# Kernel optimization log

Hardware: AMD Instinct MI355X
Metric: run time of the kernel (lower is better)

The kernel has to match this reference:

```python
import jax, jax.numpy as jnp
import numpy as np
from jax import lax

B, N, C, H = 8, 1024, 384, 6
D = C // H
SCALE = D ** -0.5
EPS = 1e-5


def setup_inputs() -> dict:
    key = jax.random.key(0)
    ks = jax.random.split(key, 10)
    s = 0.02
    return {
        "x": jax.random.normal(ks[0], (B, N, C), jnp.float32),
        "w_qkv": jax.random.normal(ks[1], (3 * C, C), jnp.float32) * s,
        "w_proj": jax.random.normal(ks[2], (C, C), jnp.float32) * s,
        "b_proj": jax.random.normal(ks[3], (C,), jnp.float32) * s,
        "w_kq": jax.random.normal(ks[4], (H, 1, 3, 3), jnp.float32) * 0.1,   # depthwise (groups=H)
        "b_kq": jax.random.normal(ks[5], (H,), jnp.float32) * 0.1,
        "w_head": jax.random.normal(ks[6], (H, H, 1, 1), jnp.float32) * 0.1,  # 1x1 head-mixing conv
        "b_head": jax.random.normal(ks[7], (H,), jnp.float32) * 0.1,
        "gn_w": jnp.ones((H,), jnp.float32),
        "gn_b": jnp.zeros((H,), jnp.float32),
    }


def reference(x, w_qkv, w_proj, b_proj, w_kq, b_kq, w_head, b_head, gn_w, gn_b):
    # qkv projection (torch Linear: y = x @ W.T)
    qkv = (x @ w_qkv.T).reshape(B, N, 3, H, D).transpose(2, 0, 3, 1, 4)  # [3,B,H,N,D]
    q, k, v = qkv[0], qkv[1], qkv[2]

    # attention logits [B,H,N,N]
    logits = jnp.einsum("bhnd,bhmd->bhnm", q, k) * SCALE

    # depthwise (groups=H) 3x3 conv over the NxN logit map
    logits = lax.conv_general_dilated(
        logits, w_kq, window_strides=(1, 1), padding=((1, 1), (1, 1)),
        dimension_numbers=("NCHW", "OIHW", "NCHW"), feature_group_count=H,
    ) + b_kq[None, :, None, None]

    attn = jax.nn.softmax(logits, axis=-1)

    # 1x1 conv mixing heads
    attn = jnp.einsum("oh,bhnm->bonm", w_head[:, :, 0, 0], attn) + b_head[None, :, None, None]

    # GroupNorm(num_groups=H, channels=H): per (b, head) stats over NxN
    mean = attn.mean(axis=(2, 3), keepdims=True)
    var = ((attn - mean) ** 2).mean(axis=(2, 3), keepdims=True)
    attn = (attn - mean) * lax.rsqrt(var + EPS)
    attn = attn * gn_w[None, :, None, None] + gn_b[None, :, None, None]

    out = jnp.einsum("bhnm,bhmd->bhnd", attn, v)
    out = out.transpose(0, 2, 1, 3).reshape(B, N, C)
    return out @ w_proj.T + b_proj
```

## Files before the change

### kernel.cpp

```cpp
#include <hip/hip_runtime.h>

typedef unsigned short u16;
typedef __attribute__((ext_vector_type(8))) short short8;
typedef __attribute__((ext_vector_type(4))) float f32x4;

#define MFMA(a, b, c) __builtin_amdgcn_mfma_f32_16x16x32_bf16((a), (b), (c), 0, 0, 0)

__device__ inline float bf2f(u16 u) {
  union { unsigned int i; float f; } w; w.i = ((unsigned int)u) << 16; return w.f;
}
__device__ inline u16 f2bf(float x) {
  union { float f; unsigned int i; } u; u.f = x;
  unsigned int r = u.i + 0x7fffu + ((u.i >> 16) & 1u);
  return (u16)(r >> 16);
}
__device__ inline unsigned int pk2(float a, float b) {
  return (unsigned int)f2bf(a) | ((unsigned int)f2bf(b) << 16);
}
__device__ inline void unpack8(uint4 v, float* f) {
  union { unsigned int i; float g; } c;
  c.i = v.x << 16;          f[0] = c.g;
  c.i = v.x & 0xffff0000u;  f[1] = c.g;
  c.i = v.y << 16;          f[2] = c.g;
  c.i = v.y & 0xffff0000u;  f[3] = c.g;
  c.i = v.z << 16;          f[4] = c.g;
  c.i = v.z & 0xffff0000u;  f[5] = c.g;
  c.i = v.w << 16;          f[6] = c.g;
  c.i = v.w & 0xffff0000u;  f[7] = c.g;
}

static const size_t SZ_QKV = (size_t)48 * 1024 * 64 * 2;
static const size_t SZ_MAP = (size_t)48 * 1024 * 1024 * 2;
static const size_t OFF_Q  = 0;
static const size_t OFF_K  = OFF_Q + SZ_QKV;
static const size_t OFF_VT = OFF_K + SZ_QKV;
static const size_t OFF_S  = OFF_VT + SZ_QKV;
static const size_t OFF_UG = OFF_S;
static const size_t OFF_QM = OFF_S + SZ_MAP;
static const size_t OFF_OT = OFF_QM + SZ_MAP;
static const size_t OFF_ST = OFF_OT + SZ_QKV;
static const size_t OFF_CS = OFF_ST + 896;
static const size_t OFF_AD = OFF_CS + 12288;
static const size_t OFF_AL = OFF_AD + 12288;

__global__ __launch_bounds__(256, 3) void k_qkv(const float* __restrict__ x,
                                                const float* __restrict__ w,
                                                u16* __restrict__ qb,
                                                u16* __restrict__ kb,
                                                u16* __restrict__ vT,
                                                float* __restrict__ colsum) {
  __shared__ u16 SH[16384];
  u16* As = SH;
  u16* Bs = SH + 8192;
  const int t = threadIdx.x;
  const int m0 = blockIdx.x * 128;
  const int n0 = blockIdx.y * 128;
  const int wave = t >> 6, lane = t & 63;
  const int wm = (wave & 1) * 64, wn = (wave >> 1) * 64;
  const int fr = lane & 15;
  const int fk = (lane >> 4) * 8;
  f32x4 acc[4][4] = {};
  for (int k0 = 0; k0 < 384; k0 += 64) {
#pragma unroll
    for (int i = 0; i < 4; ++i) {
      int e = (i * 256 + t) * 8;
      int row = e >> 6, col = e & 63;
      const float* xp = &x[(size_t)(m0 + row) * 384 + k0 + col];
      const float* wp = &w[(size_t)(n0 + row) * 384 + k0 + col];
      float4 a0 = *(const float4*)xp, a1 = *(const float4*)(xp + 4);
      uint4 av; av.x = pk2(a0.x, a0.y); av.y = pk2(a0.z, a0.w);
      av.z = pk2(a1.x, a1.y); av.w = pk2(a1.z, a1.w);
      *(uint4*)&As[e] = av;
      float4 b0 = *(const float4*)wp, b1 = *(const float4*)(wp + 4);
      uint4 bv; bv.x = pk2(b0.x, b0.y); bv.y = pk2(b0.z, b0.w);
      bv.z = pk2(b1.x, b1.y); bv.w = pk2(b1.z, b1.w);
      *(uint4*)&Bs[e] = bv;
    }
    __syncthreads();
#pragma unroll
    for (int ks = 0; ks < 2; ++ks) {
      const int ko = ks * 32 + fk;
      short8 a[4], b[4];
#pragma unroll
      for (int mi = 0; mi < 4; ++mi) a[mi] = *(const short8*)&As[(wm + mi * 16 + fr) * 64 + ko];
#pragma unroll
      for (int ni = 0; ni < 4; ++ni) b[ni] = *(const short8*)&Bs[(wn + ni * 16 + fr) * 64 + ko];
#pragma unroll
      for (int mi = 0; mi < 4; ++mi)
#pragma unroll
        for (int ni = 0; ni < 4; ++ni) acc[mi][ni] = MFMA(a[mi], b[ni], acc[mi][ni]);
    }
    __syncthreads();
  }
  u16* st = &SH[wave * 4096];
  const int gcb = n0 + wn;
  const int s = gcb / 384;
  const int remb = gcb - s * 384;
  const int h = remb >> 6;
#pragma unroll
  for (int mi = 0; mi < 4; ++mi)
#pragma unroll
    for (int ni = 0; ni < 4; ++ni)
#pragma unroll
      for (int r = 0; r < 4; ++r) {
        int rl = mi * 16 + (lane >> 4) * 4 + r;
        int cl = ni * 16 + fr;
        u16 val = f2bf(acc[mi][ni][r]);
        if (s == 2) st[cl * 64 + rl] = val;
        else        st[rl * 64 + cl] = val;
      }
  const int gm0 = m0 + wm;
  const int b_ = gm0 >> 10;
  const size_t base = (size_t)(b_ * 6 + h) << 16;
  const int nloc = gm0 & 1023;
  const int r8 = lane >> 3, c8 = (lane & 7) * 8;
#pragma unroll
  for (int i = 0; i < 8; ++i) {
    int lrow = i * 8 + r8;
    uint4 v = *(const uint4*)&st[lrow * 64 + c8];
    if (s == 0)      *(uint4*)&qb[base + (size_t)(nloc + lrow) * 64 + c8] = v;
    else if (s == 1) *(uint4*)&kb[base + (size_t)(nloc + lrow) * 64 + c8] = v;
    else             *(uint4*)&vT[base + (size_t)lrow * 1024 + nloc + c8] = v;
  }
  if (s == 2) {
#pragma unroll
    for (int ni = 0; ni < 4; ++ni) {
      float p = 0.f;
#pragma unroll
      for (int mi = 0; mi < 4; ++mi)
#pragma unroll
        for (int r = 0; r < 4; ++r) p += bf2f(f2bf(acc[mi][ni][r]));
      p += __shfl_xor(p, 16, 64);
      p += __shfl_xor(p, 32, 64);
      if ((lane >> 4) == 0)
        atomicAdd(&colsum[(b_ * 6 + h) * 64 + ni * 16 + fr], p);
    }
  }
}

__global__ __launch_bounds__(256, 3) void k_qk(const u16* __restrict__ qb,
                                               const u16* __restrict__ kb,
                                               u16* __restrict__ S) {
  __shared__ u16 SH[16384];
  u16* As = SH;
  u16* Bs = SH + 8192;
  const int t = threadIdx.x;
  const int m0 = blockIdx.x * 128, n0 = blockIdx.y * 128;
  const int bh = blockIdx.z;
  const u16* A = qb + ((size_t)bh << 16);
  const u16* Bp = kb + ((size_t)bh << 16);
  const int wave = t >> 6, lane = t & 63;
  const int wm = (wave & 1) * 64, wn = (wave >> 1) * 64;
  const int fr = lane & 15;
  const int fk = (lane >> 4) * 8;
  f32x4 acc[4][4] = {};
#pragma unroll
  for (int i = 0; i < 4; ++i) {
    int e = (i * 256 + t) * 8;
    *(uint4*)&As[e] = *(const uint4*)&A[(size_t)m0 * 64 + e];
    *(uint4*)&Bs[e] = *(const uint4*)&Bp[(size_t)n0 * 64 + e];
  }
  __syncthreads();
#pragma unroll
  for (int ks = 0; ks < 2; ++ks) {
    const int ko = ks * 32 + fk;
    short8 a[4], b[4];
#pragma unroll
    for (int mi = 0; mi < 4; ++mi) a[mi] = *(const short8*)&As[(wm + mi * 16 + fr) * 64 + ko];
#pragma unroll
    for (int ni = 0; ni < 4; ++ni) b[ni] = *(const short8*)&Bs[(wn + ni * 16 + fr) * 64 + ko];
#pragma unroll
    for (int mi = 0; mi < 4; ++mi)
#pragma unroll
      for (int ni = 0; ni < 4; ++ni) acc[mi][ni] = MFMA(a[mi], b[ni], acc[mi][ni]);
  }
  __syncthreads();
  u16* st = &SH[wave * 4096];
#pragma unroll
  for (int mi = 0; mi < 4; ++mi)
#pragma unroll
    for (int ni = 0; ni < 4; ++ni)
#pragma unroll
      for (int r = 0; r < 4; ++r)
        st[(mi * 16 + (lane >> 4) * 4 + r) * 64 + ni * 16 + fr] = f2bf(acc[mi][ni][r] * 0.125f);
  const size_t sb = (size_t)bh << 20;
  const int grow0 = m0 + wm, gcol0 = n0 + wn;
  const int r8 = lane >> 3, c8 = (lane & 7) * 8;
#pragma unroll
  for (int i = 0; i < 8; ++i) {
    int lrow = i * 8 + r8;
    uint4 v = *(const uint4*)&st[lrow * 64 + c8];
    *(uint4*)&S[sb + (size_t)(grow0 + lrow) * 1024 + gcol0 + c8] = v;
  }
}

__global__ __launch_bounds__(256) void k_conv_softmax(const u16* __restrict__ S,
                                                      const float* __restrict__ w_kq,
                                                      u16* __restrict__ Qb) {
  __shared__ u16 Sr[10 * 1040];
  __shared__ float red[4];
  const int t = threadIdx.x;
  const int bh = blockIdx.y;
  const int h = bh % 6;
  const int r0 = blockIdx.x * 8;
  const u16* Sp = S + ((size_t)bh << 20);
  float wv[9];
#pragma unroll
  for (int i = 0; i < 9; ++i) wv[i] = w_kq[h * 9 + i];
  if (t < 10) { Sr[t * 1040 + 7] = 0; Sr[t * 1040 + 1032] = 0; }
#pragma unroll
  for (int c = 0; c < 5; ++c) {
    int e = (c * 256 + t) * 8;
    int i = e >> 10, col = e & 1023;
    int g = r0 - 1 + i;
    uint4 val = make_uint4(0u, 0u, 0u, 0u);
    if (g >= 0 && g < 1024) val = *(const uint4*)&Sp[(size_t)g * 1024 + col];
    *(uint4*)&Sr[i * 1040 + 8 + col] = val;
  }
  __syncthreads();
  const int half = t >> 7;
  const int lane = t & 63;
  const int m0 = (t & 127) * 8;
  for (int pass = 0; pass < 4; ++pass) {
    int rr = pass * 2 + half;
    float o8[8];
#pragma unroll
    for (int j = 0; j < 8; ++j) o8[j] = 0.f;
#pragma unroll
    for (int i = 0; i < 3; ++i) {
      const u16* rowp = &Sr[(rr + i) * 1040 + 8];
      float left = bf2f(rowp[m0 - 1]);
      float md[8];
      unpack8(*(const uint4*)&rowp[m0], md);
      float right = bf2f(rowp[m0 + 8]);
      float w0 = wv[i * 3 + 0], w1 = wv[i * 3 + 1], w2 = wv[i * 3 + 2];
      o8[0] += w0 * left + w1 * md[0] + w2 * md[1];
#pragma unroll
      for (int j = 1; j < 7; ++j) o8[j] += w0 * md[j - 1] + w1 * md[j] + w2 * md[j + 1];
      o8[7] += w0 * md[6] + w1 * md[7] + w2 * right;
    }
    float mx = o8[0];
#pragma unroll
    for (int j = 1; j < 8; ++j) mx = fmaxf(mx, o8[j]);
    for (int off = 32; off; off >>= 1) mx = fmaxf(mx, __shfl_xor(mx, off, 64));
    if (lane == 0) red[t >> 6] = mx;
    __syncthreads();
    float rmax = fmaxf(red[half * 2], red[half * 2 + 1]);
    __syncthreads();
    float e8[8], s = 0.f;
#pragma unroll
    for (int j = 0; j < 8; ++j) { e8[j] = __expf(o8[j] - rmax); s += e8[j]; }
    for (int off = 32; off; off >>= 1) s += __shfl_xor(s, off, 64);
    if (lane == 0) red[t >> 6] = s;
    __syncthreads();
    float rsum = red[half * 2] + red[half * 2 + 1];
    __syncthreads();
    float scale = 1024.f / rsum;
    unsigned int pk[4];
#pragma unroll
    for (int jj = 0; jj < 4; ++jj)
      pk[jj] = pk2(e8[2 * jj] * scale - 1.f, e8[2 * jj + 1] * scale - 1.f);
    int n = r0 + rr;
    *(uint4*)&Qb[((size_t)bh << 20) + (size_t)n * 1024 + m0] = make_uint4(pk[0], pk[1], pk[2], pk[3]);
  }
}

__global__ __launch_bounds__(256) void k_pvmix(const u16* __restrict__ Qm,
                                               const u16* __restrict__ vT,
                                               const float* __restrict__ wh,
                                               float* __restrict__ Ug,
                                               float* __restrict__ stats) {
  __shared__ u16 SH[2 * 64 * 72];
  u16* Am = SH;
  u16* Vm = SH + 64 * 72;
  const int t = threadIdx.x;
  const int n0 = blockIdx.x * 64;
  const int bo = blockIdx.y;
  const int b_ = bo / 6, o = bo - b_ * 6;
  const int wave = t >> 6, lane = t & 63;
  const int fr = lane & 15, quad = lane >> 4;
  const int srow = t >> 3, smg8 = (t & 7) * 8;
  float wo[6];
#pragma unroll
  for (int hh = 0; hh < 6; ++hh) wo[hh] = wh[o * 6 + hh];
  const size_t qbase = ((size_t)(b_ * 6)) << 20;
  const u16* vp = vT + ((size_t)bo << 16);
  uint4 qpre[2][6];
  uint4 vpre[2];
  {
    const int m = smg8;
#pragma unroll
    for (int i = 0; i < 2; ++i)
#pragma unroll
      for (int hh = 0; hh < 6; ++hh)
        qpre[i][hh] = *(const uint4*)&Qm[qbase + (((size_t)hh) << 20) +
                                         (size_t)(n0 + i * 32 + srow) * 1024 + m];
    vpre[0] = *(const uint4*)&vp[(size_t)srow * 1024 + m];
    vpre[1] = *(const uint4*)&vp[(size_t)(32 + srow) * 1024 + m];
  }
  f32x4 acc[4] = {};
  float s1 = 0.f, s2 = 0.f;
  for (int mc = 0; mc < 16; ++mc) {
    __syncthreads();
#pragma unroll
    for (int i = 0; i < 2; ++i) {
      float mix[8] = {0.f, 0.f, 0.f, 0.f, 0.f, 0.f, 0.f, 0.f};
#pragma unroll
      for (int hh = 0; hh < 6; ++hh) {
        float qf[8];
        unpack8(qpre[i][hh], qf);
        float w = wo[hh];
#pragma unroll
        for (int j = 0; j < 8; ++j) mix[j] += w * qf[j];
      }
#pragma unroll
      for (int j = 0; j < 8; ++j) { s1 += mix[j]; s2 += mix[j] * mix[j]; }
      uint4 pk4;
      pk4.x = pk2(mix[0], mix[1]); pk4.y = pk2(mix[2], mix[3]);
      pk4.z = pk2(mix[4], mix[5]); pk4.w = pk2(mix[6], mix[7]);
      *(uint4*)&Am[(i * 32 + srow) * 72 + smg8] = pk4;
    }
    *(uint4*)&Vm[srow * 72 + smg8] = vpre[0];
    *(uint4*)&Vm[(32 + srow) * 72 + smg8] = vpre[1];
    if (mc < 15) {
      const int m = (mc + 1) * 64 + smg8;
#pragma unroll
      for (int i = 0; i < 2; ++i)
#pragma unroll
        for (int hh = 0; hh < 6; ++hh)
          qpre[i][hh] = *(const uint4*)&Qm[qbase + (((size_t)hh) << 20) +
                                           (size_t)(n0 + i * 32 + srow) * 1024 + m];
      vpre[0] = *(const uint4*)&vp[(size_t)srow * 1024 + m];
      vpre[1] = *(const uint4*)&vp[(size_t)(32 + srow) * 1024 + m];
    }
    __syncthreads();
#pragma unroll
    for (int ks = 0; ks < 2; ++ks) {
      short8 a = *(const short8*)&Am[(wave * 16 + fr) * 72 + ks * 32 + quad * 8];
#pragma unroll
      for (int ni = 0; ni < 4; ++ni) {
        short8 b = *(const short8*)&Vm[(ni * 16 + fr) * 72 + ks * 32 + quad * 8];
        acc[ni] = MFMA(a, b, acc[ni]);
      }
    }
  }
  __syncthreads();
  float* FS = (float*)SH;
#pragma unroll
  for (int ni = 0; ni < 4; ++ni)
#pragma unroll
    for (int r = 0; r < 4; ++r)
      FS[(wave * 16 + quad * 4 + r) * 64 + ni * 16 + fr] = acc[ni][r];
  __syncthreads();
  float* Up = Ug + ((size_t)(bo * 1024 + n0)) * 64;
#pragma unroll
  for (int j = 0; j < 4; ++j) {
    int oo = j * 1024 + t * 4;
    *(float4*)&Up[oo] = *(const float4*)&FS[oo];
  }
  for (int off = 32; off; off >>= 1) {
    s1 += __shfl_xor(s1, off, 64);
    s2 += __shfl_xor(s2, off, 64);
  }
  if (lane == 0) {
    atomicAdd(&stats[bo * 2 + 0], s1);
    atomicAdd(&stats[bo * 2 + 1], s2);
  }
}

__global__ __launch_bounds__(256) void k_finalize(const float* __restrict__ stats,
                                                  const float* __restrict__ colsum,
                                                  const float* __restrict__ gn_w,
                                                  const float* __restrict__ gn_b,
                                                  float* __restrict__ addend,
                                                  float* __restrict__ alphaArr) {
  int gid = blockIdx.x * 256 + threadIdx.x;
  int bo = gid >> 6, d = gid & 63;
  int o = bo % 6;
  float s1 = stats[bo * 2], s2 = stats[bo * 2 + 1];
  const float inv = 1.f / 1048576.f;
  float mu = s1 * inv;
  float var = s2 * inv - mu * mu;
  float alpha = gn_w[o] * rsqrtf(var + 1e-5f * 1048576.f);
  float beta = gn_b[o] - alpha * mu;
  addend[gid] = beta * colsum[gid];
  if (d == 0) alphaArr[bo] = alpha;
}

__global__ __launch_bounds__(256) void k_apply(const float* __restrict__ Ug,
                                               const float* __restrict__ alphaArr,
                                               const float* __restrict__ addend,
                                               u16* __restrict__ otmp) {
  int i = blockIdx.x * 256 + threadIdx.x;
  int e = i * 4;
  int d4 = e & 63;
  int n = (e >> 6) & 1023;
  int bo = e >> 16;
  float al = alphaArr[bo];
  const float* ap = &addend[bo * 64 + d4];
  float4 u = *(const float4*)&Ug[e];
  int b = bo / 6, o = bo - b * 6;
  uint2 w;
  w.x = pk2(al * u.x + ap[0], al * u.y + ap[1]);
  w.y = pk2(al * u.z + ap[2], al * u.w + ap[3]);
  *(uint2*)&otmp[((size_t)(b * 1024 + n)) * 384 + o * 64 + d4] = w;
}

__global__ __launch_bounds__(256, 3) void k_proj(const u16* __restrict__ A,
                                                 const float* __restrict__ w,
                                                 const float* __restrict__ bias,
                                                 float* __restrict__ out) {
  __shared__ u16 SH[16384];
  u16* As = SH;
  u16* Bs = SH + 8192;
  const int t = threadIdx.x;
  const int m0 = blockIdx.x * 128;
  const int n0 = blockIdx.y * 128;
  const int wave = t >> 6, lane = t & 63;
  const int wm = (wave & 1) * 64, wn = (wave >> 1) * 64;
  const int fr = lane & 15;
  const int fk = (lane >> 4) * 8;
  f32x4 acc[4][4] = {};
  for (int k0 = 0; k0 < 384; k0 += 64) {
#pragma unroll
    for (int i = 0; i < 4; ++i) {
      int e = (i * 256 + t) * 8;
      int row = e >> 6, col = e & 63;
      *(uint4*)&As[e] = *(const uint4*)&A[(size_t)(m0 + row) * 384 + k0 + col];
      const float* wp = &w[(size_t)(n0 + row) * 384 + k0 + col];
      float4 b0 = *(const float4*)wp, b1 = *(const float4*)(wp + 4);
      uint4 bv; bv.x = pk2(b0.x, b0.y); bv.y = pk2(b0.z, b0.w);
      bv.z = pk2(b1.x, b1.y); bv.w = pk2(b1.z, b1.w);
      *(uint4*)&Bs[e] = bv;
    }
    __syncthreads();
#pragma unroll
    for (int ks = 0; ks < 2; ++ks) {
      const int ko = ks * 32 + fk;
      short8 a[4], b[4];
#pragma unroll
      for (int mi = 0; mi < 4; ++mi) a[mi] = *(const short8*)&As[(wm + mi * 16 + fr) * 64 + ko];
#pragma unroll
      for (int ni = 0; ni < 4; ++ni) b[ni] = *(const short8*)&Bs[(wn + ni * 16 + fr) * 64 + ko];
#pragma unroll
      for (int mi = 0; mi < 4; ++mi)
#pragma unroll
        for (int ni = 0; ni < 4; ++ni) acc[mi][ni] = MFMA(a[mi], b[ni], acc[mi][ni]);
    }
    __syncthreads();
  }
  float* FS = (float*)SH;
  float* fst = &FS[wave * 2048];
  float bv[4];
#pragma unroll
  for (int ni = 0; ni < 4; ++ni) bv[ni] = bias[n0 + wn + ni * 16 + fr];
#pragma unroll
  for (int half = 0; half < 2; ++half) {
#pragma unroll
    for (int mi2 = 0; mi2 < 2; ++mi2) {
      int mi = half * 2 + mi2;
#pragma unroll
      for (int ni = 0; ni < 4; ++ni)
#pragma unroll
        for (int r = 0; r < 4; ++r)
          fst[(mi2 * 16 + (lane >> 4) * 4 + r) * 64 + ni * 16 + fr] = acc[mi][ni][r] + bv[ni];
    }
#pragma unroll
    for (int g = 0; g < 4; ++g)
#pragma unroll
      for (int i2 = 0; i2 < 2; ++i2) {
        int lrow = g * 8 + (lane >> 3);
        int colf = i2 * 32 + (lane & 7) * 4;
        float4 v = *(const float4*)&fst[lrow * 64 + colf];
        *(float4*)&out[(size_t)(m0 + wm + half * 32 + lrow) * 384 + n0 + wn + colf] = v;
      }
  }
}

extern "C" void kernel_launch(void* const* d_in, const int* in_sizes, int n_in,
                              void* d_out, int out_size, void* d_ws, size_t ws_size,
                              hipStream_t stream) {
  (void)in_sizes; (void)n_in; (void)out_size; (void)ws_size;
  const float* x      = (const float*)d_in[0];
  const float* w_qkv  = (const float*)d_in[1];
  const float* w_proj = (const float*)d_in[2];
  const float* b_proj = (const float*)d_in[3];
  const float* w_kq   = (const float*)d_in[4];
  const float* w_head = (const float*)d_in[6];
  const float* gn_w   = (const float*)d_in[8];
  const float* gn_b   = (const float*)d_in[9];

  char* ws = (char*)d_ws;
  u16*   qb      = (u16*)(ws + OFF_Q);
  u16*   kb      = (u16*)(ws + OFF_K);
  u16*   vT      = (u16*)(ws + OFF_VT);
  u16*   Sb      = (u16*)(ws + OFF_S);
  float* Ug      = (float*)(ws + OFF_UG);
  u16*   Qm      = (u16*)(ws + OFF_QM);
  u16*   otmp    = (u16*)(ws + OFF_OT);
  float* stats   = (float*)(ws + OFF_ST);
  float* colsum  = (float*)(ws + OFF_CS);
  float* addend  = (float*)(ws + OFF_AD);
  float* alphaA  = (float*)(ws + OFF_AL);

  hipMemsetAsync(stats, 0, 896 + 12288, stream);
  k_qkv<<<dim3(64, 9), 256, 0, stream>>>(x, w_qkv, qb, kb, vT, colsum);
  k_qk<<<dim3(8, 8, 48), 256, 0, stream>>>(qb, kb, Sb);
  k_conv_softmax<<<dim3(128, 48), 256, 0, stream>>>(Sb, w_kq, Qm);
  k_pvmix<<<dim3(16, 48), 256, 0, stream>>>(Qm, vT, w_head, Ug, stats);
  k_finalize<<<dim3(12), 256, 0, stream>>>(stats, colsum, gn_w, gn_b, addend, alphaA);
  k_apply<<<dim3(3072), 256, 0, stream>>>(Ug, alphaA, addend, otmp);
  k_proj<<<dim3(64, 3), 256, 0, stream>>>(otmp, w_proj, b_proj, (float*)d_out);
}
```

Baseline: 286.5 us.

## Compute two output heads per PV-mix block and fold GroupNorm finalize into apply

The head-mix plus PV kernel now has each block produce two output heads over 32 query rows. The six-head attention map rows it loads from global memory are therefore mixed twice and reused, which halves the re-reading of the large Qm map across output heads. The separate finalize kernel is removed and the apply kernel computes alpha and beta from the stats directly, saving one launch and a round trip through global memory. In exchange each block holds two V tiles in shared memory and uses more registers, and the grid shape changes.

```diff
diff --git a/kernel.cpp b/kernel.cpp
--- a/kernel.cpp
+++ b/kernel.cpp
@@ -40,8 +40,6 @@
 static const size_t OFF_OT = OFF_QM + SZ_MAP;
 static const size_t OFF_ST = OFF_OT + SZ_QKV;
 static const size_t OFF_CS = OFF_ST + 896;
-static const size_t OFF_AD = OFF_CS + 12288;
-static const size_t OFF_AL = OFF_AD + 12288;
 
 __global__ __launch_bounds__(256, 3) void k_qkv(const float* __restrict__ x,
                                                 const float* __restrict__ w,
@@ -265,81 +263,95 @@
   }
 }
 
-__global__ __launch_bounds__(256) void k_pvmix(const u16* __restrict__ Qm,
-                                               const u16* __restrict__ vT,
-                                               const float* __restrict__ wh,
-                                               float* __restrict__ Ug,
-                                               float* __restrict__ stats) {
-  __shared__ u16 SH[2 * 64 * 72];
-  u16* Am = SH;
-  u16* Vm = SH + 64 * 72;
+__global__ __launch_bounds__(256) void k_pvmix2(const u16* __restrict__ Qm,
+                                                const u16* __restrict__ vT,
+                                                const float* __restrict__ wh,
+                                                float* __restrict__ Ug,
+                                                float* __restrict__ stats) {
+  __shared__ u16 SH[13056];
   const int t = threadIdx.x;
-  const int n0 = blockIdx.x * 64;
-  const int bo = blockIdx.y;
-  const int b_ = bo / 6, o = bo - b_ * 6;
+  const int n0 = blockIdx.x * 32;
+  const int by = blockIdx.y;
+  const int b_ = by / 3, op = by - b_ * 3;
+  const int bo0 = b_ * 6 + op * 2;
   const int wave = t >> 6, lane = t & 63;
   const int fr = lane & 15, quad = lane >> 4;
+  const int oo = wave >> 1, rb = wave & 1;
   const int srow = t >> 3, smg8 = (t & 7) * 8;
-  float wo[6];
-#pragma unroll
-  for (int hh = 0; hh < 6; ++hh) wo[hh] = wh[o * 6 + hh];
+  float wo0[6], wo1[6];
+#pragma unroll
+  for (int hh = 0; hh < 6; ++hh) {
+    wo0[hh] = wh[(op * 2 + 0) * 6 + hh];
+    wo1[hh] = wh[(op * 2 + 1) * 6 + hh];
+  }
   const size_t qbase = ((size_t)(b_ * 6)) << 20;
-  const u16* vp = vT + ((size_t)bo << 16);
-  uint4 qpre[2][6];
-  uint4 vpre[2];
+  const u16* vp0 = vT + ((size_t)bo0 << 16);
+  const u16* vp1 = vT + ((size_t)(bo0 + 1) << 16);
+  uint4 qpre[6], vpre0[2], vpre1[2];
   {
     const int m = smg8;
 #pragma unroll
-    for (int i = 0; i < 2; ++i)
-#pragma unroll
-      for (int hh = 0; hh < 6; ++hh)
-        qpre[i][hh] = *(const uint4*)&Qm[qbase + (((size_t)hh) << 20) +
-                                         (size_t)(n0 + i * 32 + srow) * 1024 + m];
-    vpre[0] = *(const uint4*)&vp[(size_t)srow * 1024 + m];
-    vpre[1] = *(const uint4*)&vp[(size_t)(32 + srow) * 1024 + m];
+    for (int hh = 0; hh < 6; ++hh)
+      qpre[hh] = *(const uint4*)&Qm[qbase + (((size_t)hh) << 20) + (size_t)(n0 + srow) * 1024 + m];
+#pragma unroll
+    for (int i = 0; i < 2; ++i) {
+      vpre0[i] = *(const uint4*)&vp0[(size_t)(i * 32 + srow) * 1024 + m];
+      vpre1[i] = *(const uint4*)&vp1[(size_t)(i * 32 + srow) * 1024 + m];
+    }
   }
   f32x4 acc[4] = {};
-  float s1 = 0.f, s2 = 0.f;
+  float s1o0 = 0.f, s2o0 = 0.f, s1o1 = 0.f, s2o1 = 0.f;
   for (int mc = 0; mc < 16; ++mc) {
     __syncthreads();
-#pragma unroll
-    for (int i = 0; i < 2; ++i) {
-      float mix[8] = {0.f, 0.f, 0.f, 0.f, 0.f, 0.f, 0.f, 0.f};
+    {
+      float mix0[8] = {0.f, 0.f, 0.f, 0.f, 0.f, 0.f, 0.f, 0.f};
+      float mix1[8] = {0.f, 0.f, 0.f, 0.f, 0.f, 0.f, 0.f, 0.f};
 #pragma unroll
       for (int hh = 0; hh < 6; ++hh) {
         float qf[8];
-        unpack8(qpre[i][hh], qf);
-        float w = wo[hh];
-#pragma unroll
-        for (int j = 0; j < 8; ++j) mix[j] += w * qf[j];
+        unpack8(qpre[hh], qf);
+        float w0 = wo0[hh], w1 = wo1[hh];
+#pragma unroll
+        for (int j = 0; j < 8; ++j) { mix0[j] += w0 * qf[j]; mix1[j] += w1 * qf[j]; }
       }
 #pragma unroll
-      for (int j = 0; j < 8; ++j) { s1 += mix[j]; s2 += mix[j] * mix[j]; }
-      uint4 pk4;
-      pk4.x = pk2(mix[0], mix[1]); pk4.y = pk2(mix[2], mix[3]);
-      pk4.z = pk2(mix[4], mix[5]); pk4.w = pk2(mix[6], mix[7]);
-      *(uint4*)&Am[(i * 32 + srow) * 72 + smg8] = pk4;
-    }
-    *(uint4*)&Vm[srow * 72 + smg8] = vpre[0];
-    *(uint4*)&Vm[(32 + srow) * 72 + smg8] = vpre[1];
+      for (int j = 0; j < 8; ++j) {
+        s1o0 += mix0[j]; s2o0 += mix0[j] * mix0[j];
+        s1o1 += mix1[j]; s2o1 += mix1[j] * mix1[j];
+      }
+      uint4 p0, p1;
+      p0.x = pk2(mix0[0], mix0[1]); p0.y = pk2(mix0[2], mix0[3]);
+      p0.z = pk2(mix0[4], mix0[5]); p0.w = pk2(mix0[6], mix0[7]);
+      p1.x = pk2(mix1[0], mix1[1]); p1.y = pk2(mix1[2], mix1[3]);
+      p1.z = pk2(mix1[4], mix1[5]); p1.w = pk2(mix1[6], mix1[7]);
+      *(uint4*)&SH[srow * 68 + smg8] = p0;
+      *(uint4*)&SH[2176 + srow * 68 + smg8] = p1;
+    }
+#pragma unroll
+    for (int i = 0; i < 2; ++i) {
+      *(uint4*)&SH[4352 + (i * 32 + srow) * 68 + smg8] = vpre0[i];
+      *(uint4*)&SH[8704 + (i * 32 + srow) * 68 + smg8] = vpre1[i];
+    }
     if (mc < 15) {
       const int m = (mc + 1) * 64 + smg8;
 #pragma unroll
-      for (int i = 0; i < 2; ++i)
-#pragma unroll
-        for (int hh = 0; hh < 6; ++hh)
-          qpre[i][hh] = *(const uint4*)&Qm[qbase + (((size_t)hh) << 20) +
-                                           (size_t)(n0 + i * 32 + srow) * 1024 + m];
-      vpre[0] = *(const uint4*)&vp[(size_t)srow * 1024 + m];
-      vpre[1] = *(const uint4*)&vp[(size_t)(32 + srow) * 1024 + m];
-    }
-    __syncthreads();
+      for (int hh = 0; hh < 6; ++hh)
+        qpre[hh] = *(const uint4*)&Qm[qbase + (((size_t)hh) << 20) + (size_t)(n0 + srow) * 1024 + m];
+#pragma unroll
+      for (int i = 0; i < 2; ++i) {
+        vpre0[i] = *(const uint4*)&vp0[(size_t)(i * 32 + srow) * 1024 + m];
+        vpre1[i] = *(const uint4*)&vp1[(size_t)(i * 32 + srow) * 1024 + m];
+      }
+    }
+    __syncthreads();
+    const u16* Amw = SH + oo * 2176;
+    const u16* Vmw = SH + 4352 + oo * 4352;
 #pragma unroll
     for (int ks = 0; ks < 2; ++ks) {
-      short8 a = *(const short8*)&Am[(wave * 16 + fr) * 72 + ks * 32 + quad * 8];
+      short8 a = *(const short8*)&Amw[(rb * 16 + fr) * 68 + ks * 32 + quad * 8];
 #pragma unroll
       for (int ni = 0; ni < 4; ++ni) {
-        short8 b = *(const short8*)&Vm[(ni * 16 + fr) * 72 + ks * 32 + quad * 8];
+        short8 b = *(const short8*)&Vmw[(ni * 16 + fr) * 68 + ks * 32 + quad * 8];
         acc[ni] = MFMA(a, b, acc[ni]);
       }
     }
@@ -350,59 +362,53 @@
   for (int ni = 0; ni < 4; ++ni)
 #pragma unroll
     for (int r = 0; r < 4; ++r)
-      FS[(wave * 16 + quad * 4 + r) * 64 + ni * 16 + fr] = acc[ni][r];
+      FS[oo * 2048 + (rb * 16 + quad * 4 + r) * 64 + ni * 16 + fr] = acc[ni][r];
   __syncthreads();
-  float* Up = Ug + ((size_t)(bo * 1024 + n0)) * 64;
-#pragma unroll
-  for (int j = 0; j < 4; ++j) {
-    int oo = j * 1024 + t * 4;
-    *(float4*)&Up[oo] = *(const float4*)&FS[oo];
+  float* Up0 = Ug + ((size_t)(bo0 * 1024 + n0)) * 64;
+  float* Up1 = Ug + ((size_t)((bo0 + 1) * 1024 + n0)) * 64;
+#pragma unroll
+  for (int j = 0; j < 2; ++j) {
+    int idx = (j * 256 + t) * 4;
+    *(float4*)&Up0[idx] = *(const float4*)&FS[idx];
+    *(float4*)&Up1[idx] = *(const float4*)&FS[2048 + idx];
   }
   for (int off = 32; off; off >>= 1) {
-    s1 += __shfl_xor(s1, off, 64);
-    s2 += __shfl_xor(s2, off, 64);
+    s1o0 += __shfl_xor(s1o0, off, 64);
+    s2o0 += __shfl_xor(s2o0, off, 64);
+    s1o1 += __shfl_xor(s1o1, off, 64);
+    s2o1 += __shfl_xor(s2o1, off, 64);
   }
   if (lane == 0) {
-    atomicAdd(&stats[bo * 2 + 0], s1);
-    atomicAdd(&stats[bo * 2 + 1], s2);
-  }
-}
-
-__global__ __launch_bounds__(256) void k_finalize(const float* __restrict__ stats,
-                                                  const float* __restrict__ colsum,
-                                                  const float* __restrict__ gn_w,
-                                                  const float* __restrict__ gn_b,
-                                                  float* __restrict__ addend,
-                                                  float* __restrict__ alphaArr) {
-  int gid = blockIdx.x * 256 + threadIdx.x;
-  int bo = gid >> 6, d = gid & 63;
-  int o = bo % 6;
+    atomicAdd(&stats[bo0 * 2 + 0], s1o0);
+    atomicAdd(&stats[bo0 * 2 + 1], s2o0);
+    atomicAdd(&stats[(bo0 + 1) * 2 + 0], s1o1);
+    atomicAdd(&stats[(bo0 + 1) * 2 + 1], s2o1);
+  }
+}
+
+__global__ __launch_bounds__(256) void k_apply(const float* __restrict__ Ug,
+                                               const float* __restrict__ stats,
+                                               const float* __restrict__ colsum,
+                                               const float* __restrict__ gn_w,
+                                               const float* __restrict__ gn_b,
+                                               u16* __restrict__ otmp) {
+  int i = blockIdx.x * 256 + threadIdx.x;
+  int e = i * 4;
+  int d4 = e & 63;
+  int n = (e >> 6) & 1023;
+  int bo = e >> 16;
+  int b = bo / 6, o = bo - b * 6;
   float s1 = stats[bo * 2], s2 = stats[bo * 2 + 1];
   const float inv = 1.f / 1048576.f;
   float mu = s1 * inv;
   float var = s2 * inv - mu * mu;
   float alpha = gn_w[o] * rsqrtf(var + 1e-5f * 1048576.f);
   float beta = gn_b[o] - alpha * mu;
-  addend[gid] = beta * colsum[gid];
-  if (d == 0) alphaArr[bo] = alpha;
-}
-
-__global__ __launch_bounds__(256) void k_apply(const float* __restrict__ Ug,
-                                               const float* __restrict__ alphaArr,
-                                               const float* __restrict__ addend,
-                                               u16* __restrict__ otmp) {
-  int i = blockIdx.x * 256 + threadIdx.x;
-  int e = i * 4;
-  int d4 = e & 63;
-  int n = (e >> 6) & 1023;
-  int bo = e >> 16;
-  float al = alphaArr[bo];
-  const float* ap = &addend[bo * 64 + d4];
+  float4 cs = *(const float4*)&colsum[bo * 64 + d4];
   float4 u = *(const float4*)&Ug[e];
-  int b = bo / 6, o = bo - b * 6;
   uint2 w;
-  w.x = pk2(al * u.x + ap[0], al * u.y + ap[1]);
-  w.y = pk2(al * u.z + ap[2], al * u.w + ap[3]);
+  w.x = pk2(alpha * u.x + beta * cs.x, alpha * u.y + beta * cs.y);
+  w.y = pk2(alpha * u.z + beta * cs.z, alpha * u.w + beta * cs.w);
   *(uint2*)&otmp[((size_t)(b * 1024 + n)) * 384 + o * 64 + d4] = w;
 }
 
@@ -500,15 +506,12 @@
   u16*   otmp    = (u16*)(ws + OFF_OT);
   float* stats   = (float*)(ws + OFF_ST);
   float* colsum  = (float*)(ws + OFF_CS);
-  float* addend  = (float*)(ws + OFF_AD);
-  float* alphaA  = (float*)(ws + OFF_AL);
 
   hipMemsetAsync(stats, 0, 896 + 12288, stream);
   k_qkv<<<dim3(64, 9), 256, 0, stream>>>(x, w_qkv, qb, kb, vT, colsum);
   k_qk<<<dim3(8, 8, 48), 256, 0, stream>>>(qb, kb, Sb);
   k_conv_softmax<<<dim3(128, 48), 256, 0, stream>>>(Sb, w_kq, Qm);
-  k_pvmix<<<dim3(16, 48), 256, 0, stream>>>(Qm, vT, w_head, Ug, stats);
-  k_finalize<<<dim3(12), 256, 0, stream>>>(stats, colsum, gn_w, gn_b, addend, alphaA);
-  k_apply<<<dim3(3072), 256, 0, stream>>>(Ug, alphaA, addend, otmp);
+  k_pvmix2<<<dim3(32, 24), 256, 0, stream>>>(Qm, vT, w_head, Ug, stats);
+  k_apply<<<dim3(3072), 256, 0, stream>>>(Ug, stats, colsum, gn_w, gn_b, otmp);
   k_proj<<<dim3(64, 3), 256, 0, stream>>>(otmp, w_proj, b_proj, (float*)d_out);
 }
```

Result: slower. 340.9 us (+19.0%).
